# Performance work log

Measured on AMD Instinct MI355X. Metric: run time of the kernel, lower is better.

## Reference

```python
import jax, jax.numpy as jnp
import numpy as np

N, L, HID = 8192, 256, 128   # rows, input_len, hidden_size
H, NLIN = 2, 2               # n_heads, n_linear
EPS = 1e-5


def setup_inputs() -> dict:
    key = jax.random.key(0)
    ks = jax.random.split(key, 8)
    # attention params (torch.randn in source; scaled 0.02 for numerical sanity of softmax logits)
    Q = jax.random.normal(ks[0], (H, L, HID), jnp.float32) * 0.02
    K = jax.random.normal(ks[1], (H, L, HID), jnp.float32) * 0.02
    V_down = jax.random.normal(ks[2], (H, L, HID), jnp.float32) * 0.02
    V_up = jax.random.normal(ks[3], (H, HID, L), jnp.float32) * 0.02
    # nn.Linear(input_len, input_len): uniform(-1/sqrt(L), 1/sqrt(L))
    bnd = 1.0 / np.sqrt(L)
    W = jax.random.uniform(ks[4], (NLIN, L, L), jnp.float32, -bnd, bnd)
    b = jax.random.uniform(ks[5], (NLIN, L), jnp.float32, -bnd, bnd)
    x = jax.random.normal(ks[6], (N, L), jnp.float32)
    return {"x": x, "Q": Q, "K": K, "V_down": V_down, "V_up": V_up, "W": W, "b": b}


def _batch_norm(z):
    # custom BatchNorm1d: per-feature normalization over the batch (row) dim, no affine
    m = jnp.mean(z, axis=0, keepdims=True)
    v = jnp.var(z, axis=0, keepdims=True)
    return (z - m) * jax.lax.rsqrt(v + EPS)


def reference(x, Q, K, V_down, V_up, W, b):
    h = _batch_norm(x)                              # [N, L]
    dE = jnp.zeros_like(h)
    for i in range(Q.shape[0]):                     # small fixed head count
        q = h @ Q[i]                                # [N, HID]
        k = h @ K[i]                                # [N, HID]
        A = jax.nn.softmax(q @ k.T, axis=1)         # [N, N]
        dE = dE + A @ (h @ V_down[i]) @ V_up[i]     # low-rank value path
    h = _batch_norm(h + dE)
    for j in range(W.shape[0]):                     # per-row Linear+ReLU loop == batched matmul
        h = jax.nn.relu(h @ W[j].T + b[j])
    return h
```

## Files before the change

kernel.cpp:

```cpp
#include <hip/hip_runtime.h>
#include <hip/hip_bf16.h>

constexpr int Nrows = 8192;
constexpr int L     = 256;
constexpr int D     = 128;
constexpr float EPS = 1e-5f;

typedef __bf16 bf16x8 __attribute__((ext_vector_type(8)));
typedef __bf16 bf16x4 __attribute__((ext_vector_type(4)));
typedef float  f32x4  __attribute__((ext_vector_type(4)));

#define MFMA16(a, b, c) __builtin_amdgcn_mfma_f32_16x16x32_bf16((a), (b), (c), 0, 0, 0)

__global__ void k_cvt_params(const float* __restrict__ Q, const float* __restrict__ K,
                             const float* __restrict__ Vd, const float* __restrict__ Vup,
                             const float* __restrict__ W,
                             __bf16* __restrict__ Bt, __bf16* __restrict__ VupT,
                             __bf16* __restrict__ Wb) {
    int i = blockIdx.x * 256 + threadIdx.x;
    if (i < 6 * 128 * 256) {
        int g = i >> 15; int r = i & 32767; int d = r >> 8; int l = r & 255;
        const float* src = (g % 3 == 0 ? Q : (g % 3 == 1 ? K : Vd)) + (g / 3) * (L * D);
        Bt[i] = (__bf16)src[l * D + d];
    } else if (i < 8 * 128 * 256) {
        int j = i - 6 * 128 * 256;
        int h = j >> 15; int r = j & 32767; int l = r >> 7; int d = r & 127;
        VupT[j] = (__bf16)Vup[h * (D * L) + d * L + l];
    } else {
        int j = i - 8 * 128 * 256;
        Wb[j] = (__bf16)W[j];
    }
}

__global__ void k_bn_stats(const float* __restrict__ x, float* __restrict__ sum,
                           float* __restrict__ sq) {
    int col = threadIdx.x;
    int r0 = blockIdx.x * 64;
    float s = 0.f, s2 = 0.f;
    for (int i = 0; i < 64; i++) {
        float v = x[(r0 + i) * L + col];
        s += v; s2 += v * v;
    }
    atomicAdd(&sum[col], s);
    atomicAdd(&sq[col], s2);
}

__global__ void k_bn_norm1(const float* __restrict__ x, const float* __restrict__ sum,
                           const float* __restrict__ sq, __bf16* __restrict__ hb,
                           float* __restrict__ hf) {
    int i = (blockIdx.x * 256 + threadIdx.x) * 4;
    int col = i & (L - 1);
    f32x4 v = *(const f32x4*)(x + i);
    bf16x4 o; f32x4 of;
#pragma unroll
    for (int j = 0; j < 4; j++) {
        float m   = sum[col + j] * (1.0f / Nrows);
        float var = sq[col + j] * (1.0f / Nrows) - m * m;
        float rs  = rsqrtf(var + EPS);
        float t = (v[j] - m) * rs;
        of[j] = t; o[j] = (__bf16)t;
    }
    *(bf16x4*)(hb + i) = o;
    *(f32x4*)(hf + i) = of;
}

__global__ void k_bn_norm2(const float* __restrict__ z, const float* __restrict__ sum,
                           const float* __restrict__ sq, __bf16* __restrict__ h) {
    int i = (blockIdx.x * 256 + threadIdx.x) * 4;
    int col = i & (L - 1);
    f32x4 v = *(const f32x4*)(z + i);
    bf16x4 o;
#pragma unroll
    for (int j = 0; j < 4; j++) {
        float m   = sum[col + j] * (1.0f / Nrows);
        float var = sq[col + j] * (1.0f / Nrows) - m * m;
        float rs  = rsqrtf(var + EPS);
        o[j] = (__bf16)((v[j] - m) * rs);
    }
    *(bf16x4*)(h + i) = o;
}

__launch_bounds__(256)
__global__ void k_gemm_qkv(const __bf16* __restrict__ h, const __bf16* __restrict__ Bt,
                           __bf16* __restrict__ q0, __bf16* __restrict__ k0,
                           __bf16* __restrict__ q1, __bf16* __restrict__ k1,
                           __bf16* __restrict__ Vt) {
    int g = blockIdx.y;
    int m0 = blockIdx.x * 128;
    int w = threadIdx.x >> 6, lane = threadIdx.x & 63;
    int c = lane & 15, qd = lane >> 4;
    int mw = m0 + w * 32;
    const __bf16* B = Bt + g * (128 * 256);

    f32x4 acc[2][8] = {};
#pragma unroll
    for (int kc = 0; kc < 8; kc++) {
        bf16x8 a0 = *(const bf16x8*)(h + (mw + c) * L + kc * 32 + qd * 8);
        bf16x8 a1 = *(const bf16x8*)(h + (mw + 16 + c) * L + kc * 32 + qd * 8);
#pragma unroll
        for (int nt = 0; nt < 8; nt++) {
            bf16x8 b = *(const bf16x8*)(B + (nt * 16 + c) * L + kc * 32 + qd * 8);
            acc[0][nt] = MFMA16(a0, b, acc[0][nt]);
            acc[1][nt] = MFMA16(a1, b, acc[1][nt]);
        }
    }
    if (g == 2 || g == 5) {
        __bf16* vt = Vt + (g / 3) * (128 * Nrows);
#pragma unroll
        for (int mt = 0; mt < 2; mt++)
#pragma unroll
            for (int nt = 0; nt < 8; nt++)
#pragma unroll
                for (int r = 0; r < 4; r++) {
                    int row = mw + mt * 16 + 4 * qd + r;
                    int colv = nt * 16 + c;
                    vt[colv * Nrows + row] = (__bf16)acc[mt][nt][r];
                }
    } else {
        __bf16* dst = (g == 0) ? q0 : (g == 1) ? k0 : (g == 3) ? q1 : k1;
#pragma unroll
        for (int mt = 0; mt < 2; mt++)
#pragma unroll
            for (int nt = 0; nt < 8; nt++)
#pragma unroll
                for (int r = 0; r < 4; r++) {
                    int row = mw + mt * 16 + 4 * qd + r;
                    int colv = nt * 16 + c;
                    dst[row * D + colv] = (__bf16)acc[mt][nt][r];
                }
    }
}

__launch_bounds__(256, 1)
__global__ void k_flash(const __bf16* __restrict__ q0, const __bf16* __restrict__ k0,
                        const __bf16* __restrict__ q1, const __bf16* __restrict__ k1,
                        const __bf16* __restrict__ Vt, __bf16* __restrict__ O) {
    int head = blockIdx.x & 1;
    int qtile = blockIdx.x >> 1;
    int m0 = qtile * 64;
    const __bf16* qm = head ? q1 : q0;
    const __bf16* km = head ? k1 : k0;
    const __bf16* vt = Vt + head * (128 * Nrows);
    __bf16* Og = O + head * (Nrows * D);

    int w = threadIdx.x >> 6, lane = threadIdx.x & 63;
    int c = lane & 15, qd = lane >> 4;

    __shared__ __bf16 Pb[4][64 * 56];
    __shared__ float l_red[4][64];
    __shared__ float l_inv[64];
    __shared__ float obuf[4][64][16];

    bf16x8 aq[4][4];
#pragma unroll
    for (int mt = 0; mt < 4; mt++)
#pragma unroll
        for (int kc = 0; kc < 4; kc++)
            aq[mt][kc] = *(const bf16x8*)(qm + (m0 + mt * 16 + c) * D + kc * 32 + qd * 8);

    f32x4 oacc[4][8] = {};
    float lp[4][4] = {};
    __bf16* Pw = &Pb[w][0];

    for (int n0 = 0; n0 < Nrows; n0 += 128) {
        int nb = n0 + w * 32;
        bf16x8 kb[2][4], vb[8];
#pragma unroll
        for (int nt = 0; nt < 2; nt++)
#pragma unroll
            for (int kc = 0; kc < 4; kc++)
                kb[nt][kc] = *(const bf16x8*)(km + (nb + nt * 16 + c) * D + kc * 32 + qd * 8);
#pragma unroll
        for (int dvt = 0; dvt < 8; dvt++)
            vb[dvt] = *(const bf16x8*)(vt + (dvt * 16 + c) * Nrows + nb + qd * 8);

#pragma unroll
        for (int nt = 0; nt < 2; nt++) {
            f32x4 s[4] = {};
#pragma unroll
            for (int kc = 0; kc < 4; kc++) {
#pragma unroll
                for (int mt = 0; mt < 4; mt++) s[mt] = MFMA16(aq[mt][kc], kb[nt][kc], s[mt]);
            }
#pragma unroll
            for (int mt = 0; mt < 4; mt++)
#pragma unroll
                for (int r = 0; r < 4; r++) {
                    float e = __expf(s[mt][r]);
                    lp[mt][r] += e;
                    Pw[(mt * 16 + 4 * qd + r) * 56 + nt * 16 + c] = (__bf16)e;
                }
        }
        bf16x8 ap[4];
#pragma unroll
        for (int mt = 0; mt < 4; mt++)
            ap[mt] = *(const bf16x8*)(Pw + (mt * 16 + c) * 56 + qd * 8);
#pragma unroll
        for (int dvt = 0; dvt < 8; dvt++) {
#pragma unroll
            for (int mt = 0; mt < 4; mt++) oacc[mt][dvt] = MFMA16(ap[mt], vb[dvt], oacc[mt][dvt]);
        }
    }

#pragma unroll
    for (int mt = 0; mt < 4; mt++)
#pragma unroll
        for (int r = 0; r < 4; r++) {
            float v = lp[mt][r];
            v += __shfl_xor(v, 1, 16);
            v += __shfl_xor(v, 2, 16);
            v += __shfl_xor(v, 4, 16);
            v += __shfl_xor(v, 8, 16);
            lp[mt][r] = v;
        }
    if (c == 0) {
#pragma unroll
        for (int mt = 0; mt < 4; mt++)
#pragma unroll
            for (int r = 0; r < 4; r++)
                l_red[w][mt * 16 + 4 * qd + r] = lp[mt][r];
    }
    __syncthreads();
    if (threadIdx.x < 64)
        l_inv[threadIdx.x] = 1.0f / (l_red[0][threadIdx.x] + l_red[1][threadIdx.x] +
                                     l_red[2][threadIdx.x] + l_red[3][threadIdx.x]);

    for (int dvt = 0; dvt < 8; dvt++) {
        __syncthreads();
#pragma unroll
        for (int mt = 0; mt < 4; mt++)
#pragma unroll
            for (int r = 0; r < 4; r++)
                obuf[w][mt * 16 + 4 * qd + r][c] = oacc[mt][dvt][r];
        __syncthreads();
        int t = threadIdx.x;
        int row = (t * 4) >> 4, col = (t * 4) & 15;
        f32x4 v = *(const f32x4*)&obuf[0][row][col];
        f32x4 v1 = *(const f32x4*)&obuf[1][row][col];
        f32x4 v2 = *(const f32x4*)&obuf[2][row][col];
        f32x4 v3 = *(const f32x4*)&obuf[3][row][col];
        float il = l_inv[row];
        bf16x4 o;
#pragma unroll
        for (int e = 0; e < 4; e++) o[e] = (__bf16)((v[e] + v1[e] + v2[e] + v3[e]) * il);
        *(bf16x4*)(Og + (m0 + row) * D + dvt * 16 + col) = o;
    }
}

__launch_bounds__(256)
__global__ void k_gemm_vup(const __bf16* __restrict__ O, const __bf16* __restrict__ VupT,
                           const float* __restrict__ hf, float* __restrict__ z) {
    int n0 = blockIdx.y * 128;
    int m0 = blockIdx.x * 128;
    int w = threadIdx.x >> 6, lane = threadIdx.x & 63;
    int c = lane & 15, qd = lane >> 4;
    int mw = m0 + w * 32;

    f32x4 acc[2][8] = {};
#pragma unroll
    for (int kc = 0; kc < 8; kc++) {
        const __bf16* Oh = O + (kc >> 2) * (Nrows * D);
        const __bf16* Vh = VupT + (kc >> 2) * (L * D);
        int ko = (kc & 3) * 32 + qd * 8;
        bf16x8 a0 = *(const bf16x8*)(Oh + (mw + c) * D + ko);
        bf16x8 a1 = *(const bf16x8*)(Oh + (mw + 16 + c) * D + ko);
#pragma unroll
        for (int nt = 0; nt < 8; nt++) {
            bf16x8 b = *(const bf16x8*)(Vh + (n0 + nt * 16 + c) * D + ko);
            acc[0][nt] = MFMA16(a0, b, acc[0][nt]);
            acc[1][nt] = MFMA16(a1, b, acc[1][nt]);
        }
    }
#pragma unroll
    for (int mt = 0; mt < 2; mt++)
#pragma unroll
        for (int nt = 0; nt < 8; nt++)
#pragma unroll
            for (int r = 0; r < 4; r++) {
                int row = mw + mt * 16 + 4 * qd + r;
                int col = n0 + nt * 16 + c;
                z[row * L + col] = acc[mt][nt][r] + hf[row * L + col];
            }
}

template <typename OutT>
__launch_bounds__(256)
__global__ void k_gemm_w(const __bf16* __restrict__ hin, const __bf16* __restrict__ W,
                         const float* __restrict__ bias, OutT* __restrict__ out) {
    int n0 = blockIdx.y * 128;
    int m0 = blockIdx.x * 128;
    int w = threadIdx.x >> 6, lane = threadIdx.x & 63;
    int c = lane & 15, qd = lane >> 4;
    int mw = m0 + w * 32;

    f32x4 acc[2][8] = {};
#pragma unroll
    for (int kc = 0; kc < 8; kc++) {
        bf16x8 a0 = *(const bf16x8*)(hin + (mw + c) * L + kc * 32 + qd * 8);
        bf16x8 a1 = *(const bf16x8*)(hin + (mw + 16 + c) * L + kc * 32 + qd * 8);
#pragma unroll
        for (int nt = 0; nt < 8; nt++) {
            bf16x8 b = *(const bf16x8*)(W + (n0 + nt * 16 + c) * L + kc * 32 + qd * 8);
            acc[0][nt] = MFMA16(a0, b, acc[0][nt]);
            acc[1][nt] = MFMA16(a1, b, acc[1][nt]);
        }
    }
#pragma unroll
    for (int mt = 0; mt < 2; mt++)
#pragma unroll
        for (int nt = 0; nt < 8; nt++) {
            int col = n0 + nt * 16 + c;
            float bv = bias[col];
#pragma unroll
            for (int r = 0; r < 4; r++) {
                int row = mw + mt * 16 + 4 * qd + r;
                float v = fmaxf(acc[mt][nt][r] + bv, 0.0f);
                out[row * L + col] = (OutT)v;
            }
        }
}

extern "C" void kernel_launch(void* const* d_in, const int* in_sizes, int n_in,
                              void* d_out, int out_size, void* d_ws, size_t ws_size,
                              hipStream_t stream) {
    (void)in_sizes; (void)n_in; (void)out_size; (void)ws_size;
    const float* x   = (const float*)d_in[0];
    const float* Q   = (const float*)d_in[1];
    const float* K   = (const float*)d_in[2];
    const float* Vd  = (const float*)d_in[3];
    const float* Vup = (const float*)d_in[4];
    const float* W   = (const float*)d_in[5];
    const float* b   = (const float*)d_in[6];
    float* out = (float*)d_out;

    char* ws = (char*)d_ws;
    size_t off = 0;
    auto alloc = [&](size_t bytes) -> void* {
        void* p = ws + off;
        off += (bytes + 255) & ~(size_t)255;
        return p;
    };
    float*  stats = (float*)alloc(4 * 256 * sizeof(float));
    __bf16* Bt    = (__bf16*)alloc(6 * 128 * 256 * 2);
    __bf16* VupT  = (__bf16*)alloc(2 * 256 * 128 * 2);
    __bf16* Wb    = (__bf16*)alloc(2 * 256 * 256 * 2);
    __bf16* hb    = (__bf16*)alloc((size_t)Nrows * L * 2);
    float*  hf    = (float*)alloc((size_t)Nrows * L * 4);
    __bf16* q0    = (__bf16*)alloc((size_t)Nrows * D * 2);
    __bf16* k0    = (__bf16*)alloc((size_t)Nrows * D * 2);
    __bf16* q1    = (__bf16*)alloc((size_t)Nrows * D * 2);
    __bf16* k1    = (__bf16*)alloc((size_t)Nrows * D * 2);
    __bf16* Vt    = (__bf16*)alloc((size_t)2 * 128 * Nrows * 2);
    __bf16* O     = (__bf16*)alloc((size_t)2 * Nrows * D * 2);
    float*  z     = (float*)alloc((size_t)Nrows * L * 4);
    __bf16* h2    = (__bf16*)alloc((size_t)Nrows * L * 2);
    __bf16* h3    = (__bf16*)alloc((size_t)Nrows * L * 2);

    float* sum1 = stats, *sq1 = stats + 256, *sum2 = stats + 512, *sq2 = stats + 768;

    hipMemsetAsync(stats, 0, 4 * 256 * sizeof(float), stream);
    k_cvt_params<<<1536, 256, 0, stream>>>(Q, K, Vd, Vup, W, Bt, VupT, Wb);
    k_bn_stats<<<128, 256, 0, stream>>>(x, sum1, sq1);
    k_bn_norm1<<<2048, 256, 0, stream>>>(x, sum1, sq1, hb, hf);
    k_gemm_qkv<<<dim3(64, 6), 256, 0, stream>>>(hb, Bt, q0, k0, q1, k1, Vt);
    k_flash<<<256, 256, 0, stream>>>(q0, k0, q1, k1, Vt, O);
    k_gemm_vup<<<dim3(64, 2), 256, 0, stream>>>(O, VupT, hf, z);
    k_bn_stats<<<128, 256, 0, stream>>>(z, sum2, sq2);
    k_bn_norm2<<<2048, 256, 0, stream>>>(z, sum2, sq2, h2);
    k_gemm_w<__bf16><<<dim3(64, 2), 256, 0, stream>>>(h2, Wb, b, h3);
    k_gemm_w<float><<<dim3(64, 2), 256, 0, stream>>>(h3, Wb + 256 * 256, b + 256, out);
}
```

Baseline: 328.4 us.

## Split attention key range into segments with partial sums and combine kernel

The flash attention kernel now splits the key dimension into four segments across a second grid dimension. Each block writes unnormalized fp32 partial outputs and partial softmax denominators, and a new combine kernel sums them and normalizes to bf16. Launch bounds are raised to allow more blocks per CU, shared buffers are aliased to cut LDS use, and the stats memset is folded into the parameter conversion kernel. This is meant to raise occupancy and CU utilization, at the cost of extra global memory traffic for the partial buffers and one more launch.

After: 627.8 us. 1.91x slower.

```diff
diff --git a/kernel.cpp b/kernel.cpp
--- a/kernel.cpp
+++ b/kernel.cpp
@@ -5,6 +5,8 @@
 constexpr int L     = 256;
 constexpr int D     = 128;
 constexpr float EPS = 1e-5f;
+constexpr int NSEG  = 4;
+constexpr int SEGK  = Nrows / NSEG;
 
 typedef __bf16 bf16x8 __attribute__((ext_vector_type(8)));
 typedef __bf16 bf16x4 __attribute__((ext_vector_type(4)));
@@ -16,7 +18,11 @@
                              const float* __restrict__ Vd, const float* __restrict__ Vup,
                              const float* __restrict__ W,
                              __bf16* __restrict__ Bt, __bf16* __restrict__ VupT,
-                             __bf16* __restrict__ Wb) {
+                             __bf16* __restrict__ Wb, float* __restrict__ stats) {
+    if (blockIdx.x == 0) {
+        f32x4 zz = {0.f, 0.f, 0.f, 0.f};
+        ((f32x4*)stats)[threadIdx.x] = zz;
+    }
     int i = blockIdx.x * 256 + threadIdx.x;
     if (i < 6 * 128 * 256) {
         int g = i >> 15; int r = i & 32767; int d = r >> 8; int l = r & 255;
@@ -131,25 +137,26 @@
     }
 }
 
-__launch_bounds__(256, 1)
+__launch_bounds__(256, 3)
 __global__ void k_flash(const __bf16* __restrict__ q0, const __bf16* __restrict__ k0,
                         const __bf16* __restrict__ q1, const __bf16* __restrict__ k1,
-                        const __bf16* __restrict__ Vt, __bf16* __restrict__ O) {
+                        const __bf16* __restrict__ Vt, float* __restrict__ Opart,
+                        float* __restrict__ lpart) {
     int head = blockIdx.x & 1;
     int qtile = blockIdx.x >> 1;
+    int seg = blockIdx.y;
     int m0 = qtile * 64;
     const __bf16* qm = head ? q1 : q0;
     const __bf16* km = head ? k1 : k0;
     const __bf16* vt = Vt + head * (128 * Nrows);
-    __bf16* Og = O + head * (Nrows * D);
 
     int w = threadIdx.x >> 6, lane = threadIdx.x & 63;
     int c = lane & 15, qd = lane >> 4;
 
-    __shared__ __bf16 Pb[4][64 * 56];
-    __shared__ float l_red[4][64];
-    __shared__ float l_inv[64];
-    __shared__ float obuf[4][64][16];
+    __shared__ char smem[4 * 64 * 56 * 2 + 4 * 64 * 4];
+    __bf16* Pb = (__bf16*)smem;
+    float (*obuf)[64][16] = (float (*)[64][16])smem;
+    float (*l_red)[64] = (float (*)[64])(smem + 4 * 64 * 56 * 2);
 
     bf16x8 aq[4][4];
 #pragma unroll
@@ -160,9 +167,10 @@
 
     f32x4 oacc[4][8] = {};
     float lp[4][4] = {};
-    __bf16* Pw = &Pb[w][0];
-
-    for (int n0 = 0; n0 < Nrows; n0 += 128) {
+    __bf16* Pw = Pb + w * (64 * 56);
+
+    int nbeg = seg * SEGK;
+    for (int n0 = nbeg; n0 < nbeg + SEGK; n0 += 128) {
         int nb = n0 + w * 32;
         bf16x8 kb[2][4], vb[8];
 #pragma unroll
@@ -221,10 +229,13 @@
                 l_red[w][mt * 16 + 4 * qd + r] = lp[mt][r];
     }
     __syncthreads();
-    if (threadIdx.x < 64)
-        l_inv[threadIdx.x] = 1.0f / (l_red[0][threadIdx.x] + l_red[1][threadIdx.x] +
-                                     l_red[2][threadIdx.x] + l_red[3][threadIdx.x]);
-
+    if (threadIdx.x < 64) {
+        float lt = l_red[0][threadIdx.x] + l_red[1][threadIdx.x] +
+                   l_red[2][threadIdx.x] + l_red[3][threadIdx.x];
+        lpart[(head * NSEG + seg) * Nrows + m0 + threadIdx.x] = lt;
+    }
+
+    float* Op = Opart + ((size_t)(head * NSEG + seg) * Nrows + m0) * D;
     for (int dvt = 0; dvt < 8; dvt++) {
         __syncthreads();
 #pragma unroll
@@ -235,16 +246,35 @@
         __syncthreads();
         int t = threadIdx.x;
         int row = (t * 4) >> 4, col = (t * 4) & 15;
-        f32x4 v = *(const f32x4*)&obuf[0][row][col];
+        f32x4 v  = *(const f32x4*)&obuf[0][row][col];
         f32x4 v1 = *(const f32x4*)&obuf[1][row][col];
         f32x4 v2 = *(const f32x4*)&obuf[2][row][col];
         f32x4 v3 = *(const f32x4*)&obuf[3][row][col];
-        float il = l_inv[row];
-        bf16x4 o;
-#pragma unroll
-        for (int e = 0; e < 4; e++) o[e] = (__bf16)((v[e] + v1[e] + v2[e] + v3[e]) * il);
-        *(bf16x4*)(Og + (m0 + row) * D + dvt * 16 + col) = o;
-    }
+        f32x4 o = v + v1 + v2 + v3;
+        *(f32x4*)(Op + row * D + dvt * 16 + col) = o;
+    }
+}
+
+__global__ void k_combine(const float* __restrict__ Opart, const float* __restrict__ lpart,
+                          __bf16* __restrict__ O) {
+    int t = blockIdx.x * 256 + threadIdx.x;
+    int i4 = t * 4;
+    int head = i4 >> 20;
+    int idx = i4 & (Nrows * D - 1);
+    int row = idx >> 7;
+    f32x4 s = {0.f, 0.f, 0.f, 0.f};
+    float l = 0.f;
+#pragma unroll
+    for (int sg = 0; sg < NSEG; sg++) {
+        const float* Op = Opart + (size_t)(head * NSEG + sg) * (Nrows * D);
+        s += *(const f32x4*)(Op + idx);
+        l += lpart[(head * NSEG + sg) * Nrows + row];
+    }
+    float il = 1.0f / l;
+    bf16x4 o;
+#pragma unroll
+    for (int e = 0; e < 4; e++) o[e] = (__bf16)(s[e] * il);
+    *(bf16x4*)(O + (size_t)head * (Nrows * D) + idx) = o;
 }
 
 __launch_bounds__(256)
@@ -355,15 +385,17 @@
     float*  z     = (float*)alloc((size_t)Nrows * L * 4);
     __bf16* h2    = (__bf16*)alloc((size_t)Nrows * L * 2);
     __bf16* h3    = (__bf16*)alloc((size_t)Nrows * L * 2);
+    float*  Opart = (float*)alloc((size_t)2 * NSEG * Nrows * D * 4);
+    float*  lpart = (float*)alloc((size_t)2 * NSEG * Nrows * 4);
 
     float* sum1 = stats, *sq1 = stats + 256, *sum2 = stats + 512, *sq2 = stats + 768;
 
-    hipMemsetAsync(stats, 0, 4 * 256 * sizeof(float), stream);
-    k_cvt_params<<<1536, 256, 0, stream>>>(Q, K, Vd, Vup, W, Bt, VupT, Wb);
+    k_cvt_params<<<1536, 256, 0, stream>>>(Q, K, Vd, Vup, W, Bt, VupT, Wb, stats);
     k_bn_stats<<<128, 256, 0, stream>>>(x, sum1, sq1);
     k_bn_norm1<<<2048, 256, 0, stream>>>(x, sum1, sq1, hb, hf);
     k_gemm_qkv<<<dim3(64, 6), 256, 0, stream>>>(hb, Bt, q0, k0, q1, k1, Vt);
-    k_flash<<<256, 256, 0, stream>>>(q0, k0, q1, k1, Vt, O);
+    k_flash<<<dim3(256, NSEG), 256, 0, stream>>>(q0, k0, q1, k1, Vt, Opart, lpart);
+    k_combine<<<2048, 256, 0, stream>>>(Opart, lpart, O);
     k_gemm_vup<<<dim3(64, 2), 256, 0, stream>>>(O, VupT, hf, z);
     k_bn_stats<<<128, 256, 0, stream>>>(z, sum2, sq2);
     k_bn_norm2<<<2048, 256, 0, stream>>>(z, sum2, sq2, h2);
```

## Use eight waves per flash block and fold stats zeroing into param conversion

Applied to the files above, without the earlier changes.

The flash attention kernel now runs 512 threads (8 waves) per block. Each wave handles a 32-key slice of a 256-key step, and the final cross-wave reduction sums eight partial outputs. Shared memory is unioned so the output reduction buffer aliases the P buffer. The goal is more latency hiding from extra waves on the 256-block grid, at the cost of more register pressure and a larger reduction. The separate memset of the BN stats is also replaced by zeroing inside the conversion kernel, which removes one launch.

New measurement: 355.8 us. +8.4%, slower.

```diff
diff --git a/kernel.cpp b/kernel.cpp
--- a/kernel.cpp
+++ b/kernel.cpp
@@ -16,7 +16,11 @@
                              const float* __restrict__ Vd, const float* __restrict__ Vup,
                              const float* __restrict__ W,
                              __bf16* __restrict__ Bt, __bf16* __restrict__ VupT,
-                             __bf16* __restrict__ Wb) {
+                             __bf16* __restrict__ Wb, float* __restrict__ stats) {
+    if (blockIdx.x == 0) {
+        f32x4 zz = {0.f, 0.f, 0.f, 0.f};
+        ((f32x4*)stats)[threadIdx.x] = zz;
+    }
     int i = blockIdx.x * 256 + threadIdx.x;
     if (i < 6 * 128 * 256) {
         int g = i >> 15; int r = i & 32767; int d = r >> 8; int l = r & 255;
@@ -131,7 +135,7 @@
     }
 }
 
-__launch_bounds__(256, 1)
+__launch_bounds__(512, 2)
 __global__ void k_flash(const __bf16* __restrict__ q0, const __bf16* __restrict__ k0,
                         const __bf16* __restrict__ q1, const __bf16* __restrict__ k1,
                         const __bf16* __restrict__ Vt, __bf16* __restrict__ O) {
@@ -146,10 +150,11 @@
     int w = threadIdx.x >> 6, lane = threadIdx.x & 63;
     int c = lane & 15, qd = lane >> 4;
 
-    __shared__ __bf16 Pb[4][64 * 56];
-    __shared__ float l_red[4][64];
-    __shared__ float l_inv[64];
-    __shared__ float obuf[4][64][16];
+    __shared__ char smem[8 * 64 * 56 * 2 + 8 * 64 * 4 + 64 * 4];
+    __bf16* Pb = (__bf16*)smem;
+    float (*obuf)[64][16] = (float (*)[64][16])smem;
+    float (*l_red)[64] = (float (*)[64])(smem + 8 * 64 * 56 * 2);
+    float* l_inv = (float*)(smem + 8 * 64 * 56 * 2 + 8 * 64 * 4);
 
     bf16x8 aq[4][4];
 #pragma unroll
@@ -160,9 +165,9 @@
 
     f32x4 oacc[4][8] = {};
     float lp[4][4] = {};
-    __bf16* Pw = &Pb[w][0];
-
-    for (int n0 = 0; n0 < Nrows; n0 += 128) {
+    __bf16* Pw = Pb + w * (64 * 56);
+
+    for (int n0 = 0; n0 < Nrows; n0 += 256) {
         int nb = n0 + w * 32;
         bf16x8 kb[2][4], vb[8];
 #pragma unroll
@@ -221,9 +226,12 @@
                 l_red[w][mt * 16 + 4 * qd + r] = lp[mt][r];
     }
     __syncthreads();
-    if (threadIdx.x < 64)
-        l_inv[threadIdx.x] = 1.0f / (l_red[0][threadIdx.x] + l_red[1][threadIdx.x] +
-                                     l_red[2][threadIdx.x] + l_red[3][threadIdx.x]);
+    if (threadIdx.x < 64) {
+        float lt = 0.f;
+#pragma unroll
+        for (int ww = 0; ww < 8; ww++) lt += l_red[ww][threadIdx.x];
+        l_inv[threadIdx.x] = 1.0f / lt;
+    }
 
     for (int dvt = 0; dvt < 8; dvt++) {
         __syncthreads();
@@ -234,16 +242,17 @@
                 obuf[w][mt * 16 + 4 * qd + r][c] = oacc[mt][dvt][r];
         __syncthreads();
         int t = threadIdx.x;
-        int row = (t * 4) >> 4, col = (t * 4) & 15;
-        f32x4 v = *(const f32x4*)&obuf[0][row][col];
-        f32x4 v1 = *(const f32x4*)&obuf[1][row][col];
-        f32x4 v2 = *(const f32x4*)&obuf[2][row][col];
-        f32x4 v3 = *(const f32x4*)&obuf[3][row][col];
-        float il = l_inv[row];
-        bf16x4 o;
-#pragma unroll
-        for (int e = 0; e < 4; e++) o[e] = (__bf16)((v[e] + v1[e] + v2[e] + v3[e]) * il);
-        *(bf16x4*)(Og + (m0 + row) * D + dvt * 16 + col) = o;
+        if (t < 256) {
+            int row = t >> 2, col = (t * 4) & 15;
+            f32x4 s = {0.f, 0.f, 0.f, 0.f};
+#pragma unroll
+            for (int ww = 0; ww < 8; ww++) s += *(const f32x4*)&obuf[ww][row][col];
+            float il = l_inv[row];
+            bf16x4 o;
+#pragma unroll
+            for (int e = 0; e < 4; e++) o[e] = (__bf16)(s[e] * il);
+            *(bf16x4*)(Og + (m0 + row) * D + dvt * 16 + col) = o;
+        }
     }
 }
 
@@ -358,12 +367,11 @@
 
     float* sum1 = stats, *sq1 = stats + 256, *sum2 = stats + 512, *sq2 = stats + 768;
 
-    hipMemsetAsync(stats, 0, 4 * 256 * sizeof(float), stream);
-    k_cvt_params<<<1536, 256, 0, stream>>>(Q, K, Vd, Vup, W, Bt, VupT, Wb);
+    k_cvt_params<<<1536, 256, 0, stream>>>(Q, K, Vd, Vup, W, Bt, VupT, Wb, stats);
     k_bn_stats<<<128, 256, 0, stream>>>(x, sum1, sq1);
     k_bn_norm1<<<2048, 256, 0, stream>>>(x, sum1, sq1, hb, hf);
     k_gemm_qkv<<<dim3(64, 6), 256, 0, stream>>>(hb, Bt, q0, k0, q1, k1, Vt);
-    k_flash<<<256, 256, 0, stream>>>(q0, k0, q1, k1, Vt, O);
+    k_flash<<<256, 512, 0, stream>>>(q0, k0, q1, k1, Vt, O);
     k_gemm_vup<<<dim3(64, 2), 256, 0, stream>>>(O, VupT, hf, z);
     k_bn_stats<<<128, 256, 0, stream>>>(z, sum2, sq2);
     k_bn_norm2<<<2048, 256, 0, stream>>>(z, sum2, sq2, h2);
```
